# Optimization experiments

Measured on AMD Instinct MI355X. Metric: run time of the kernel, lower is better.

Reference implementation:

```python
import jax, jax.numpy as jnp
import numpy as np

NUM_HEADS = 12
N_TOKENS = 1

def setup_inputs() -> dict:
    key = jax.random.key(0)
    ks = jax.random.split(key, 13)
    D = 768
    s = 0.02
    return {
        "x": jax.random.normal(ks[0], (64, 1025, D), jnp.float32),
        "qW": jax.random.normal(ks[1], (D, D), jnp.float32) * s,
        "qb": jax.random.normal(ks[2], (D,), jnp.float32) * s,
        "kW": jax.random.normal(ks[3], (D, D), jnp.float32) * s,
        "kb": jax.random.normal(ks[4], (D,), jnp.float32) * s,
        "vW": jax.random.normal(ks[5], (D, D), jnp.float32) * s,
        "vb": jax.random.normal(ks[6], (D,), jnp.float32) * s,
        "w1W": jax.random.normal(ks[7], (NUM_HEADS, NUM_HEADS), jnp.float32) * 0.1,
        "w1b": jax.random.normal(ks[8], (NUM_HEADS,), jnp.float32) * 0.1,
        "w2W": jax.random.normal(ks[9], (NUM_HEADS, NUM_HEADS), jnp.float32) * 0.1,
        "w2b": jax.random.normal(ks[10], (NUM_HEADS,), jnp.float32) * 0.1,
        "projW": jax.random.normal(ks[11], (D, D), jnp.float32) * s,
        "projb": jax.random.normal(ks[12], (D,), jnp.float32) * s,
    }

def reference(x, qW, qb, kW, kb, vW, vb, w1W, w1b, w2W, w2b, projW, projb):
    B, N, C = x.shape  # C == embed_dim == 768
    H = NUM_HEADS
    d = C // H
    scale = d ** -0.5
    cls = x[:, :N_TOKENS]  # [B, n, C]
    # torch Linear: y = x @ W.T + b
    q = (cls @ qW.T + qb).reshape(B, N_TOKENS, H, d).transpose(0, 2, 1, 3) * scale  # [B,H,n,d]
    k = (x @ kW.T + kb).reshape(B, N, H, d).transpose(0, 2, 1, 3)  # [B,H,N,d]
    v = (x @ vW.T + vb).reshape(B, N, H, d).transpose(0, 2, 1, 3)  # [B,H,N,d]
    attn = jnp.einsum('bhqd,bhkd->bhqk', q, k)  # [B,H,n,N]
    # talking-heads pre-softmax: linear over head dim, added residually
    attn = attn + jnp.einsum('bhqk,gh->bgqk', attn, w1W) + w1b[None, :, None, None]
    attn = jax.nn.softmax(attn, axis=-1)
    # talking-heads post-softmax
    attn = attn + jnp.einsum('bhqk,gh->bgqk', attn, w2W) + w2b[None, :, None, None]
    out = jnp.einsum('bhqk,bhkd->bhqd', attn, v)  # [B,H,n,d]
    out = out.transpose(0, 2, 1, 3).reshape(B, N_TOKENS, C)
    return out @ projW.T + projb
```

## Files before the change

kernel.cpp:

```cpp
#include <hip/hip_runtime.h>

#define B 64
#define N 1025
#define NPAD 1028
#define C 768
#define H 12
#define HD 64

__device__ __forceinline__ float wave_reduce_add(float v) {
    #pragma unroll
    for (int m = 1; m < 64; m <<= 1) v += __shfl_xor(v, m, 64);
    return v;
}

__global__ __launch_bounds__(256) void k_qproj(const float* __restrict__ x,
                                               const float* __restrict__ qW,
                                               const float* __restrict__ qb,
                                               float* __restrict__ qout) {
    __shared__ float cls[4 * C];
    int bt = blockIdx.x, ct = blockIdx.y, tid = threadIdx.x;
    for (int i = tid; i < 768; i += 256) {
        int bl = i / 192, c4 = i % 192;
        ((float4*)cls)[i] = ((const float4*)(x + (size_t)(bt * 4 + bl) * N * C))[c4];
    }
    __syncthreads();
    int w = tid >> 6, lane = tid & 63;
    int b = bt * 4 + w;
    const float* clsrow = &cls[w * C];
    for (int cl = 0; cl < 16; ++cl) {
        int c = ct * 16 + cl;
        const float4* wr = (const float4*)(qW + (size_t)c * C + lane * 12);
        const float4* xr = (const float4*)(clsrow + lane * 12);
        float acc = 0.f;
        #pragma unroll
        for (int s = 0; s < 3; ++s) {
            float4 a = wr[s], v = xr[s];
            acc += a.x * v.x + a.y * v.y + a.z * v.z + a.w * v.w;
        }
        acc = wave_reduce_add(acc);
        if (lane == 0) qout[b * C + c] = 0.125f * (acc + qb[c]);
    }
}

__global__ __launch_bounds__(256) void k_qk(const float* __restrict__ q,
                                            const float* __restrict__ kW,
                                            const float* __restrict__ kb,
                                            float* __restrict__ qk,
                                            float* __restrict__ qkb) {
    int bt = blockIdx.x, h = blockIdx.y, tid = threadIdx.x;
    if (tid < 192) {
        float4 acc[4] = {};
        #pragma unroll 4
        for (int i = 0; i < HD; ++i) {
            int row = h * HD + i;
            float4 kv = *(const float4*)(kW + (size_t)row * C + tid * 4);
            #pragma unroll
            for (int bl = 0; bl < 4; ++bl) {
                float qv = q[(bt * 4 + bl) * C + row];
                acc[bl].x += qv * kv.x; acc[bl].y += qv * kv.y;
                acc[bl].z += qv * kv.z; acc[bl].w += qv * kv.w;
            }
        }
        #pragma unroll
        for (int bl = 0; bl < 4; ++bl) {
            int b = bt * 4 + bl;
            *(float4*)(qk + ((size_t)b * H + h) * C + tid * 4) = acc[bl];
        }
    }
    int w = tid >> 6, lane = tid & 63;
    int b = bt * 4 + w;
    float v = q[b * C + h * HD + lane] * kb[h * HD + lane];
    v = wave_reduce_add(v);
    if (lane == 0) qkb[b * H + h] = v;
}

__global__ __launch_bounds__(256) void k_scores(const float* __restrict__ x,
                                                const float* __restrict__ qk,
                                                float* __restrict__ sc) {
    __shared__ float qs[12 * C];
    int tile = blockIdx.x, b = blockIdx.y, tid = threadIdx.x;
    const float4* qksrc = (const float4*)(qk + (size_t)b * H * C);
    for (int i = tid; i < 2304; i += 256) ((float4*)qs)[i] = qksrc[i];
    __syncthreads();
    int w = tid >> 6, lane = tid & 63;
    int c16 = lane & 15, r = lane >> 4;
    int rowbase = tile * 64 + w * 16 + r * 4;
    const float* xb = x + (size_t)b * N * C;
    float acc[4][12] = {};
    for (int cc = 0; cc < C; cc += 128) {
        int c0 = cc + c16 * 4, c1 = c0 + 64;
        float4 xv0[4], xv1[4];
        #pragma unroll
        for (int j = 0; j < 4; ++j) {
            int row = rowbase + j;
            const float* xr = xb + (size_t)row * C;
            xv0[j] = (row < N) ? *(const float4*)(xr + c0) : make_float4(0.f,0.f,0.f,0.f);
            xv1[j] = (row < N) ? *(const float4*)(xr + c1) : make_float4(0.f,0.f,0.f,0.f);
        }
        #pragma unroll
        for (int h = 0; h < 12; ++h) {
            float4 q0 = *(const float4*)(qs + h * C + c0);
            float4 q1 = *(const float4*)(qs + h * C + c1);
            #pragma unroll
            for (int j = 0; j < 4; ++j) {
                acc[j][h] += xv0[j].x * q0.x + xv0[j].y * q0.y +
                             xv0[j].z * q0.z + xv0[j].w * q0.w;
                acc[j][h] += xv1[j].x * q1.x + xv1[j].y * q1.y +
                             xv1[j].z * q1.z + xv1[j].w * q1.w;
            }
        }
    }
    #pragma unroll
    for (int j = 0; j < 4; ++j)
        #pragma unroll
        for (int h = 0; h < 12; ++h) {
            float v = acc[j][h];
            v += __shfl_xor(v, 1); v += __shfl_xor(v, 2);
            v += __shfl_xor(v, 4); v += __shfl_xor(v, 8);
            acc[j][h] = v;
        }
    if (c16 == 0) {
        #pragma unroll
        for (int j = 0; j < 4; ++j) {
            int row = rowbase + j;
            if (row < N) {
                #pragma unroll
                for (int h = 0; h < 12; ++h)
                    sc[((size_t)b * H + h) * NPAD + row] = acc[j][h];
            }
        }
    }
}

__global__ __launch_bounds__(256) void k_mix1(float* __restrict__ sc,
                                              const float* __restrict__ qkbias,
                                              const float* __restrict__ w1W,
                                              const float* __restrict__ w1b,
                                              float* __restrict__ mstat,
                                              float* __restrict__ sstat) {
    __shared__ float w1s[144], w1bs[12], qbs[12];
    __shared__ float red[4][12];
    __shared__ float mg[12];
    int kk = blockIdx.x, b = blockIdx.y, tid = threadIdx.x;
    int nn = (kk == 7) ? 129 : 128;
    int n = kk * 128 + tid;
    if (tid < 144) w1s[tid] = w1W[tid];
    if (tid < 12)  { w1bs[tid] = w1b[tid]; qbs[tid] = qkbias[b * 12 + tid]; }
    __syncthreads();
    bool act = tid < nn;
    float o[12];
    if (act) {
        float s_[12];
        #pragma unroll
        for (int h = 0; h < 12; ++h)
            s_[h] = sc[((size_t)b * H + h) * NPAD + n] + qbs[h];
        #pragma unroll
        for (int g = 0; g < 12; ++g) {
            float a = s_[g] + w1bs[g];
            #pragma unroll
            for (int h = 0; h < 12; ++h) a += w1s[g * 12 + h] * s_[h];
            o[g] = a;
        }
        #pragma unroll
        for (int g = 0; g < 12; ++g)
            sc[((size_t)b * H + g) * NPAD + n] = o[g];
    } else {
        #pragma unroll
        for (int g = 0; g < 12; ++g) o[g] = -3e38f;
    }
    int w = tid >> 6, lane = tid & 63;
    #pragma unroll
    for (int g = 0; g < 12; ++g) {
        float v = o[g];
        #pragma unroll
        for (int m = 1; m < 64; m <<= 1) v = fmaxf(v, __shfl_xor(v, m, 64));
        if (lane == 0) red[w][g] = v;
    }
    __syncthreads();
    if (tid < 12)
        mg[tid] = fmaxf(fmaxf(red[0][tid], red[1][tid]),
                        fmaxf(red[2][tid], red[3][tid]));
    __syncthreads();
    #pragma unroll
    for (int g = 0; g < 12; ++g) {
        float e = act ? __expf(o[g] - mg[g]) : 0.f;
        e = wave_reduce_add(e);
        if (lane == 0) red[w][g] = e;
    }
    __syncthreads();
    if (tid < 12) {
        mstat[((size_t)b * 8 + kk) * 12 + tid] = mg[tid];
        sstat[((size_t)b * 8 + kk) * 12 + tid] =
            red[0][tid] + red[1][tid] + red[2][tid] + red[3][tid];
    }
}

#define FMA4(d, s, xv) { d.x += (s) * xv.x; d.y += (s) * xv.y; d.z += (s) * xv.z; d.w += (s) * xv.w; }
__global__ __launch_bounds__(192) void k_ysum(const float* __restrict__ x,
                                              const float* __restrict__ sc,
                                              const float* __restrict__ mstat,
                                              const float* __restrict__ sstat,
                                              const float* __restrict__ w2W,
                                              const float* __restrict__ w2b,
                                              float* __restrict__ yp) {
    __shared__ float as_[129 * 12];
    __shared__ float w2s[144], w2bs[12], msh[12], ish[12];
    int k = blockIdx.x, b = blockIdx.y, tid = threadIdx.x;
    int nlo = k * 128, nn = (k == 7) ? 129 : 128;
    if (tid < 144) w2s[tid] = w2W[tid];
    if (tid < 12) {
        w2bs[tid] = w2b[tid];
        float m = -3e38f, mv[8];
        #pragma unroll
        for (int kk = 0; kk < 8; ++kk) {
            mv[kk] = mstat[((size_t)b * 8 + kk) * 12 + tid];
            m = fmaxf(m, mv[kk]);
        }
        float S = 0.f;
        #pragma unroll
        for (int kk = 0; kk < 8; ++kk)
            S += sstat[((size_t)b * 8 + kk) * 12 + tid] * __expf(mv[kk] - m);
        msh[tid] = m; ish[tid] = 1.f / S;
    }
    __syncthreads();
    if (tid < nn) {
        int n = nlo + tid;
        float p[12];
        #pragma unroll
        for (int h = 0; h < 12; ++h)
            p[h] = __expf(sc[((size_t)b * H + h) * NPAD + n] - msh[h]) * ish[h];
        #pragma unroll
        for (int g = 0; g < 12; ++g) {
            float a = p[g] + w2bs[g];
            #pragma unroll
            for (int h = 0; h < 12; ++h) a += w2s[g * 12 + h] * p[h];
            as_[tid * 12 + g] = a;
        }
    }
    __syncthreads();
    const float* xb = x + ((size_t)b * N + nlo) * C + tid * 4;
    float4 acc[12] = {};
    int n = 0;
    for (; n + 4 <= nn; n += 4) {
        float4 xv[4];
        #pragma unroll
        for (int u = 0; u < 4; ++u)
            xv[u] = *(const float4*)(xb + (size_t)(n + u) * C);
        #pragma unroll
        for (int u = 0; u < 4; ++u) {
            const float4* ar = (const float4*)(as_ + (n + u) * 12);
            float4 a0 = ar[0], a1 = ar[1], a2 = ar[2];
            FMA4(acc[0], a0.x, xv[u]); FMA4(acc[1], a0.y, xv[u]); FMA4(acc[2], a0.z, xv[u]); FMA4(acc[3], a0.w, xv[u]);
            FMA4(acc[4], a1.x, xv[u]); FMA4(acc[5], a1.y, xv[u]); FMA4(acc[6], a1.z, xv[u]); FMA4(acc[7], a1.w, xv[u]);
            FMA4(acc[8], a2.x, xv[u]); FMA4(acc[9], a2.y, xv[u]); FMA4(acc[10], a2.z, xv[u]); FMA4(acc[11], a2.w, xv[u]);
        }
    }
    for (; n < nn; ++n) {
        float4 xv = *(const float4*)(xb + (size_t)n * C);
        const float4* ar = (const float4*)(as_ + n * 12);
        float4 a0 = ar[0], a1 = ar[1], a2 = ar[2];
        FMA4(acc[0], a0.x, xv); FMA4(acc[1], a0.y, xv); FMA4(acc[2], a0.z, xv); FMA4(acc[3], a0.w, xv);
        FMA4(acc[4], a1.x, xv); FMA4(acc[5], a1.y, xv); FMA4(acc[6], a1.z, xv); FMA4(acc[7], a1.w, xv);
        FMA4(acc[8], a2.x, xv); FMA4(acc[9], a2.y, xv); FMA4(acc[10], a2.z, xv); FMA4(acc[11], a2.w, xv);
    }
    #pragma unroll
    for (int h = 0; h < 12; ++h)
        *(float4*)(yp + (((size_t)k * B + b) * H + h) * C + tid * 4) = acc[h];
}

__global__ __launch_bounds__(256) void k_zproj(const float* __restrict__ yp,
                                               const float* __restrict__ vW,
                                               const float* __restrict__ vb,
                                               const float* __restrict__ w2W,
                                               const float* __restrict__ w2b,
                                               float* __restrict__ z) {
    __shared__ float ys[4 * C];
    int bt = blockIdx.x, h = blockIdx.y, tid = threadIdx.x;
    for (int i = tid; i < 768; i += 256) {
        int bl = i / 192, c4 = i % 192;
        int b = bt * 4 + bl;
        float4 s = make_float4(0.f, 0.f, 0.f, 0.f);
        #pragma unroll
        for (int k = 0; k < 8; ++k) {
            float4 v = ((const float4*)(yp + (((size_t)k * B + b) * H + h) * C))[c4];
            s.x += v.x; s.y += v.y; s.z += v.z; s.w += v.w;
        }
        ((float4*)ys)[i] = s;
    }
    __syncthreads();
    float sv = 1.f + 1025.f * w2b[h];
    #pragma unroll
    for (int j = 0; j < 12; ++j) sv += w2W[h * 12 + j];
    int w = tid >> 6, lane = tid & 63;
    int b = bt * 4 + w;
    const float* yrow = &ys[w * C];
    for (int cl = 0; cl < 64; ++cl) {
        int c = h * 64 + cl;
        const float4* wr = (const float4*)(vW + (size_t)c * C + lane * 12);
        const float4* yr = (const float4*)(yrow + lane * 12);
        float acc = 0.f;
        #pragma unroll
        for (int s = 0; s < 3; ++s) {
            float4 a = wr[s], v = yr[s];
            acc += a.x * v.x + a.y * v.y + a.z * v.z + a.w * v.w;
        }
        acc = wave_reduce_add(acc);
        if (lane == 0) z[b * C + c] = acc + vb[c] * sv;
    }
}

__global__ __launch_bounds__(256) void k_out(const float* __restrict__ z,
                                             const float* __restrict__ pW,
                                             const float* __restrict__ pb,
                                             float* __restrict__ out) {
    __shared__ float zs[4 * C];
    int bt = blockIdx.x, ct = blockIdx.y, tid = threadIdx.x;
    for (int i = tid; i < 768; i += 256)
        ((float4*)zs)[i] = ((const float4*)(z + (size_t)bt * 4 * C))[i];
    __syncthreads();
    int w = tid >> 6, lane = tid & 63;
    int b = bt * 4 + w;
    for (int cl = 0; cl < 16; ++cl) {
        int c = ct * 16 + cl;
        const float4* wr = (const float4*)(pW + (size_t)c * C + lane * 12);
        const float4* zr = (const float4*)(zs + w * C + lane * 12);
        float acc = 0.f;
        #pragma unroll
        for (int s = 0; s < 3; ++s) {
            float4 a = wr[s], v = zr[s];
            acc += a.x * v.x + a.y * v.y + a.z * v.z + a.w * v.w;
        }
        acc = wave_reduce_add(acc);
        if (lane == 0) out[b * C + c] = acc + pb[c];
    }
}

extern "C" void kernel_launch(void* const* d_in, const int* in_sizes, int n_in,
                              void* d_out, int out_size, void* d_ws, size_t ws_size,
                              hipStream_t stream) {
    const float* x    = (const float*)d_in[0];
    const float* qW   = (const float*)d_in[1];
    const float* qb   = (const float*)d_in[2];
    const float* kW   = (const float*)d_in[3];
    const float* kb   = (const float*)d_in[4];
    const float* vW   = (const float*)d_in[5];
    const float* vb   = (const float*)d_in[6];
    const float* w1W  = (const float*)d_in[7];
    const float* w1b  = (const float*)d_in[8];
    const float* w2W  = (const float*)d_in[9];
    const float* w2b  = (const float*)d_in[10];
    const float* pW   = (const float*)d_in[11];
    const float* pb   = (const float*)d_in[12];
    float* out = (float*)d_out;

    float* ws    = (float*)d_ws;
    float* qk    = ws + 0;
    float* qkb   = ws + 589824;
    float* q     = ws + 590592;
    float* sc    = ws + 639744;
    float* yp    = ws + 1429248;
    float* z     = ws + 6147840;
    float* mstat = ws + 6196992;
    float* sstat = ws + 6203136;

    k_qproj <<<dim3(16, 48), 256, 0, stream>>>(x, qW, qb, q);
    k_qk    <<<dim3(16, 12), 256, 0, stream>>>(q, kW, kb, qk, qkb);
    k_scores<<<dim3(17, 64), 256, 0, stream>>>(x, qk, sc);
    k_mix1  <<<dim3(8, 64), 256, 0, stream>>>(sc, qkb, w1W, w1b, mstat, sstat);
    k_ysum  <<<dim3(8, 64), 192, 0, stream>>>(x, sc, mstat, sstat, w2W, w2b, yp);
    k_zproj <<<dim3(16, 12), 256, 0, stream>>>(yp, vW, vb, w2W, w2b, z);
    k_out   <<<dim3(16, 48), 256, 0, stream>>>(z, pW, pb, out);
}
```

Measured before the change: 457.9 us.

## Fuse talking-heads pre-mix and softmax stats into scores kernel; split ysum rows

Folds the k_mix1 kernel into k_scores, so the pre-softmax head mixing and the per-tile max and sum-of-exp statistics are computed from shared memory right after the scores reduction. Scores are stored row-major as [b][n][12] so they can be written and read with float4. k_ysum doubles its block to 384 threads, splitting each 128-row chunk between two thread groups and reducing their partial sums through shared memory. This removes one launch and one round trip of the score array, at the cost of a serial mixing phase on one wave per block and extra shared memory in k_ysum.

```diff
diff --git a/kernel.cpp b/kernel.cpp
--- a/kernel.cpp
+++ b/kernel.cpp
@@ -2,10 +2,10 @@
 
 #define B 64
 #define N 1025
-#define NPAD 1028
 #define C 768
 #define H 12
 #define HD 64
+#define NT 17
 
 __device__ __forceinline__ float wave_reduce_add(float v) {
     #pragma unroll
@@ -76,11 +76,19 @@
 
 __global__ __launch_bounds__(256) void k_scores(const float* __restrict__ x,
                                                 const float* __restrict__ qk,
-                                                float* __restrict__ sc) {
+                                                const float* __restrict__ qkbias,
+                                                const float* __restrict__ w1W,
+                                                const float* __restrict__ w1b,
+                                                float* __restrict__ sc,
+                                                float* __restrict__ mstat,
+                                                float* __restrict__ sstat) {
     __shared__ float qs[12 * C];
+    __shared__ float w1s[144], w1bs[12], qbs[12];
     int tile = blockIdx.x, b = blockIdx.y, tid = threadIdx.x;
     const float4* qksrc = (const float4*)(qk + (size_t)b * H * C);
     for (int i = tid; i < 2304; i += 256) ((float4*)qs)[i] = qksrc[i];
+    if (tid < 144) w1s[tid] = w1W[tid];
+    if (tid < 12)  { w1bs[tid] = w1b[tid]; qbs[tid] = qkbias[b * 12 + tid]; }
     __syncthreads();
     int w = tid >> 6, lane = tid & 63;
     int c16 = lane & 15, r = lane >> 4;
@@ -119,41 +127,21 @@
             v += __shfl_xor(v, 4); v += __shfl_xor(v, 8);
             acc[j][h] = v;
         }
+    __syncthreads();
     if (c16 == 0) {
         #pragma unroll
-        for (int j = 0; j < 4; ++j) {
-            int row = rowbase + j;
-            if (row < N) {
-                #pragma unroll
-                for (int h = 0; h < 12; ++h)
-                    sc[((size_t)b * H + h) * NPAD + row] = acc[j][h];
-            }
-        }
-    }
-}
-
-__global__ __launch_bounds__(256) void k_mix1(float* __restrict__ sc,
-                                              const float* __restrict__ qkbias,
-                                              const float* __restrict__ w1W,
-                                              const float* __restrict__ w1b,
-                                              float* __restrict__ mstat,
-                                              float* __restrict__ sstat) {
-    __shared__ float w1s[144], w1bs[12], qbs[12];
-    __shared__ float red[4][12];
-    __shared__ float mg[12];
-    int kk = blockIdx.x, b = blockIdx.y, tid = threadIdx.x;
-    int nn = (kk == 7) ? 129 : 128;
-    int n = kk * 128 + tid;
-    if (tid < 144) w1s[tid] = w1W[tid];
-    if (tid < 12)  { w1bs[tid] = w1b[tid]; qbs[tid] = qkbias[b * 12 + tid]; }
-    __syncthreads();
-    bool act = tid < nn;
-    float o[12];
-    if (act) {
-        float s_[12];
-        #pragma unroll
-        for (int h = 0; h < 12; ++h)
-            s_[h] = sc[((size_t)b * H + h) * NPAD + n] + qbs[h];
+        for (int j = 0; j < 4; ++j)
+            #pragma unroll
+            for (int h = 0; h < 12; ++h)
+                qs[(w * 16 + r * 4 + j) * 12 + h] = acc[j][h];
+    }
+    __syncthreads();
+    if (tid < 64) {
+        int row = tile * 64 + tid;
+        bool valid = row < N;
+        float s_[12], o[12];
+        #pragma unroll
+        for (int h = 0; h < 12; ++h) s_[h] = qs[tid * 12 + h] + qbs[h];
         #pragma unroll
         for (int g = 0; g < 12; ++g) {
             float a = s_[g] + w1bs[g];
@@ -161,42 +149,29 @@
             for (int h = 0; h < 12; ++h) a += w1s[g * 12 + h] * s_[h];
             o[g] = a;
         }
-        #pragma unroll
-        for (int g = 0; g < 12; ++g)
-            sc[((size_t)b * H + g) * NPAD + n] = o[g];
-    } else {
-        #pragma unroll
-        for (int g = 0; g < 12; ++g) o[g] = -3e38f;
-    }
-    int w = tid >> 6, lane = tid & 63;
-    #pragma unroll
-    for (int g = 0; g < 12; ++g) {
-        float v = o[g];
-        #pragma unroll
-        for (int m = 1; m < 64; m <<= 1) v = fmaxf(v, __shfl_xor(v, m, 64));
-        if (lane == 0) red[w][g] = v;
-    }
-    __syncthreads();
-    if (tid < 12)
-        mg[tid] = fmaxf(fmaxf(red[0][tid], red[1][tid]),
-                        fmaxf(red[2][tid], red[3][tid]));
-    __syncthreads();
-    #pragma unroll
-    for (int g = 0; g < 12; ++g) {
-        float e = act ? __expf(o[g] - mg[g]) : 0.f;
-        e = wave_reduce_add(e);
-        if (lane == 0) red[w][g] = e;
-    }
-    __syncthreads();
-    if (tid < 12) {
-        mstat[((size_t)b * 8 + kk) * 12 + tid] = mg[tid];
-        sstat[((size_t)b * 8 + kk) * 12 + tid] =
-            red[0][tid] + red[1][tid] + red[2][tid] + red[3][tid];
+        if (valid) {
+            float* sp = sc + ((size_t)b * N + row) * 12;
+            *(float4*)(sp)     = make_float4(o[0], o[1], o[2],  o[3]);
+            *(float4*)(sp + 4) = make_float4(o[4], o[5], o[6],  o[7]);
+            *(float4*)(sp + 8) = make_float4(o[8], o[9], o[10], o[11]);
+        }
+        #pragma unroll
+        for (int g = 0; g < 12; ++g) {
+            float mv = valid ? o[g] : -3e38f;
+            #pragma unroll
+            for (int m = 1; m < 64; m <<= 1) mv = fmaxf(mv, __shfl_xor(mv, m, 64));
+            float e = valid ? __expf(o[g] - mv) : 0.f;
+            e = wave_reduce_add(e);
+            if (tid == 0) {
+                mstat[((size_t)b * NT + tile) * 12 + g] = mv;
+                sstat[((size_t)b * NT + tile) * 12 + g] = e;
+            }
+        }
     }
 }
 
 #define FMA4(d, s, xv) { d.x += (s) * xv.x; d.y += (s) * xv.y; d.z += (s) * xv.z; d.w += (s) * xv.w; }
-__global__ __launch_bounds__(192) void k_ysum(const float* __restrict__ x,
+__global__ __launch_bounds__(384) void k_ysum(const float* __restrict__ x,
                                               const float* __restrict__ sc,
                                               const float* __restrict__ mstat,
                                               const float* __restrict__ sstat,
@@ -204,31 +179,45 @@
                                               const float* __restrict__ w2b,
                                               float* __restrict__ yp) {
     __shared__ float as_[129 * 12];
+    __shared__ float4 redv[192 * 12];
     __shared__ float w2s[144], w2bs[12], msh[12], ish[12];
     int k = blockIdx.x, b = blockIdx.y, tid = threadIdx.x;
     int nlo = k * 128, nn = (k == 7) ? 129 : 128;
     if (tid < 144) w2s[tid] = w2W[tid];
     if (tid < 12) {
         w2bs[tid] = w2b[tid];
-        float m = -3e38f, mv[8];
-        #pragma unroll
-        for (int kk = 0; kk < 8; ++kk) {
-            mv[kk] = mstat[((size_t)b * 8 + kk) * 12 + tid];
+        float m = -3e38f, mv[NT];
+        #pragma unroll
+        for (int kk = 0; kk < NT; ++kk) {
+            mv[kk] = mstat[((size_t)b * NT + kk) * 12 + tid];
             m = fmaxf(m, mv[kk]);
         }
         float S = 0.f;
         #pragma unroll
-        for (int kk = 0; kk < 8; ++kk)
-            S += sstat[((size_t)b * 8 + kk) * 12 + tid] * __expf(mv[kk] - m);
+        for (int kk = 0; kk < NT; ++kk)
+            S += sstat[((size_t)b * NT + kk) * 12 + tid] * __expf(mv[kk] - m);
         msh[tid] = m; ish[tid] = 1.f / S;
     }
     __syncthreads();
     if (tid < nn) {
         int n = nlo + tid;
+        const float* sp = sc + ((size_t)b * N + n) * 12;
+        float4 s0 = *(const float4*)(sp);
+        float4 s1 = *(const float4*)(sp + 4);
+        float4 s2 = *(const float4*)(sp + 8);
         float p[12];
-        #pragma unroll
-        for (int h = 0; h < 12; ++h)
-            p[h] = __expf(sc[((size_t)b * H + h) * NPAD + n] - msh[h]) * ish[h];
+        p[0]  = __expf(s0.x - msh[0])  * ish[0];
+        p[1]  = __expf(s0.y - msh[1])  * ish[1];
+        p[2]  = __expf(s0.z - msh[2])  * ish[2];
+        p[3]  = __expf(s0.w - msh[3])  * ish[3];
+        p[4]  = __expf(s1.x - msh[4])  * ish[4];
+        p[5]  = __expf(s1.y - msh[5])  * ish[5];
+        p[6]  = __expf(s1.z - msh[6])  * ish[6];
+        p[7]  = __expf(s1.w - msh[7])  * ish[7];
+        p[8]  = __expf(s2.x - msh[8])  * ish[8];
+        p[9]  = __expf(s2.y - msh[9])  * ish[9];
+        p[10] = __expf(s2.z - msh[10]) * ish[10];
+        p[11] = __expf(s2.w - msh[11]) * ish[11];
         #pragma unroll
         for (int g = 0; g < 12; ++g) {
             float a = p[g] + w2bs[g];
@@ -238,10 +227,13 @@
         }
     }
     __syncthreads();
-    const float* xb = x + ((size_t)b * N + nlo) * C + tid * 4;
+    int grp = tid / 192, t = tid - grp * 192;
+    int n0   = grp ? 64 : 0;
+    int nend = grp ? nn : 64;
+    const float* xb = x + ((size_t)b * N + nlo) * C + t * 4;
     float4 acc[12] = {};
-    int n = 0;
-    for (; n + 4 <= nn; n += 4) {
+    int n = n0;
+    for (; n + 4 <= nend; n += 4) {
         float4 xv[4];
         #pragma unroll
         for (int u = 0; u < 4; ++u)
@@ -255,7 +247,7 @@
             FMA4(acc[8], a2.x, xv[u]); FMA4(acc[9], a2.y, xv[u]); FMA4(acc[10], a2.z, xv[u]); FMA4(acc[11], a2.w, xv[u]);
         }
     }
-    for (; n < nn; ++n) {
+    for (; n < nend; ++n) {
         float4 xv = *(const float4*)(xb + (size_t)n * C);
         const float4* ar = (const float4*)(as_ + n * 12);
         float4 a0 = ar[0], a1 = ar[1], a2 = ar[2];
@@ -263,9 +255,21 @@
         FMA4(acc[4], a1.x, xv); FMA4(acc[5], a1.y, xv); FMA4(acc[6], a1.z, xv); FMA4(acc[7], a1.w, xv);
         FMA4(acc[8], a2.x, xv); FMA4(acc[9], a2.y, xv); FMA4(acc[10], a2.z, xv); FMA4(acc[11], a2.w, xv);
     }
-    #pragma unroll
-    for (int h = 0; h < 12; ++h)
-        *(float4*)(yp + (((size_t)k * B + b) * H + h) * C + tid * 4) = acc[h];
+    if (grp == 1) {
+        #pragma unroll
+        for (int h = 0; h < 12; ++h) redv[t * 12 + h] = acc[h];
+    }
+    __syncthreads();
+    if (grp == 0) {
+        #pragma unroll
+        for (int h = 0; h < 12; ++h) {
+            float4 rv = redv[t * 12 + h];
+            acc[h].x += rv.x; acc[h].y += rv.y; acc[h].z += rv.z; acc[h].w += rv.w;
+        }
+        #pragma unroll
+        for (int h = 0; h < 12; ++h)
+            *(float4*)(yp + (((size_t)k * B + b) * H + h) * C + t * 4) = acc[h];
+    }
 }
 
 __global__ __launch_bounds__(256) void k_zproj(const float* __restrict__ yp,
@@ -358,16 +362,15 @@
     float* qkb   = ws + 589824;
     float* q     = ws + 590592;
     float* sc    = ws + 639744;
-    float* yp    = ws + 1429248;
-    float* z     = ws + 6147840;
-    float* mstat = ws + 6196992;
-    float* sstat = ws + 6203136;
+    float* yp    = ws + 1426944;
+    float* z     = ws + 6145536;
+    float* mstat = ws + 6194688;
+    float* sstat = ws + 6207744;
 
     k_qproj <<<dim3(16, 48), 256, 0, stream>>>(x, qW, qb, q);
     k_qk    <<<dim3(16, 12), 256, 0, stream>>>(q, kW, kb, qk, qkb);
-    k_scores<<<dim3(17, 64), 256, 0, stream>>>(x, qk, sc);
-    k_mix1  <<<dim3(8, 64), 256, 0, stream>>>(sc, qkb, w1W, w1b, mstat, sstat);
-    k_ysum  <<<dim3(8, 64), 192, 0, stream>>>(x, sc, mstat, sstat, w2W, w2b, yp);
+    k_scores<<<dim3(17, 64), 256, 0, stream>>>(x, qk, qkb, w1W, w1b, sc, mstat, sstat);
+    k_ysum  <<<dim3(8, 64), 384, 0, stream>>>(x, sc, mstat, sstat, w2W, w2b, yp);
     k_zproj <<<dim3(16, 12), 256, 0, stream>>>(yp, vW, vb, w2W, w2b, z);
     k_out   <<<dim3(16, 48), 256, 0, stream>>>(z, pW, pb, out);
 }
```

New measurement: 454.9 us. No clear change (-0.6%).
